# Kernel tuning notes

Hardware: AMD Instinct MI355X
Metric: run time of the kernel (lower is better)

## Reference

```python
import jax, jax.numpy as jnp
import numpy as np

EPS = 1e-5
GROUPS = 8


def setup_inputs() -> dict:
    key = jax.random.key(0)
    ks = jax.random.split(key, 6)
    C = 512
    B, H, W = 4, 64, 64
    s = 1.0 / np.sqrt(C)
    return {
        "x": jax.random.normal(ks[0], (B, C, H, W), dtype=jnp.float32),
        "gn_gamma": jnp.ones((C,), jnp.float32),
        "gn_beta": jnp.zeros((C,), jnp.float32),
        "wq": jax.random.normal(ks[1], (C, C), jnp.float32) * s,
        "bq": jnp.zeros((C,), jnp.float32),
        "wk": jax.random.normal(ks[2], (C, C), jnp.float32) * s,
        "bk": jnp.zeros((C,), jnp.float32),
        "wv": jax.random.normal(ks[3], (C, C), jnp.float32) * s,
        "bv": jnp.zeros((C,), jnp.float32),
        "wp": jax.random.normal(ks[4], (C, C), jnp.float32) * s,
        "bp": jnp.zeros((C,), jnp.float32),
    }


def _group_norm(x, gamma, beta):
    b, c, h, w = x.shape
    xg = x.reshape(b, GROUPS, c // GROUPS, h, w)
    mu = xg.mean(axis=(2, 3, 4), keepdims=True)
    var = xg.var(axis=(2, 3, 4), keepdims=True)
    xn = ((xg - mu) * jax.lax.rsqrt(var + EPS)).reshape(b, c, h, w)
    return xn * gamma[None, :, None, None] + beta[None, :, None, None]


def _conv1x1(x, w, b):
    # 1x1 conv == channel-mixing matmul: [O,C] x [B,C,H,W] -> [B,O,H,W]
    return jnp.einsum('oc,bchw->bohw', w, x) + b[None, :, None, None]


def reference(x, gn_gamma, gn_beta, wq, bq, wk, bk, wv, bv, wp, bp):
    b, c, h, w = x.shape
    xn = _group_norm(x, gn_gamma, gn_beta)  # note: residual uses normalized x, as in source
    q = _conv1x1(xn, wq, bq).reshape(b, c, h * w)
    k = _conv1x1(xn, wk, bk).reshape(b, c, h * w)
    v = _conv1x1(xn, wv, bv).reshape(b, c, h * w)
    scale = jnp.asarray(c, x.dtype) ** 0.5
    attn = jnp.einsum('bci,bcj->bij', q, k) / scale  # [b, hw, hw]
    attn = jax.nn.softmax(attn, axis=2)
    out = jnp.einsum('bij,bcj->bci', attn, v).reshape(b, c, h, w)
    out = _conv1x1(out, wp, bp)
    return xn + out
```

## Files before the change

### kernel.cpp

```cpp
#include <hip/hip_runtime.h>
#include <hip/hip_bf16.h>


typedef unsigned short u16;
typedef unsigned char u8;
typedef __bf16 bf16x8 __attribute__((ext_vector_type(8)));
typedef float f32x4 __attribute__((ext_vector_type(4)));
typedef int i32x4 __attribute__((ext_vector_type(4)));
typedef int i32x8 __attribute__((ext_vector_type(8)));
typedef unsigned short u16x4 __attribute__((ext_vector_type(4)));
typedef unsigned short u16x8 __attribute__((ext_vector_type(8)));

#define CDIM 512
#define NPOS 4096
#define NBATCH 4

__device__ __forceinline__ u16 f2bf(float x) {
  union { float f; unsigned u; } c; c.f = x;
  unsigned u = c.u;
  u += 0x7fffu + ((u >> 16) & 1u);
  return (u16)(u >> 16);
}
__device__ __forceinline__ float bf2f(u16 h) {
  union { unsigned u; float f; } c; c.u = ((unsigned)h) << 16;
  return c.f;
}
__device__ __forceinline__ unsigned pk4_fp8(float a, float b, float c, float d) {
  unsigned v = __builtin_amdgcn_cvt_pk_fp8_f32(a, b, 0, false);
  v = __builtin_amdgcn_cvt_pk_fp8_f32(c, d, v, true);
  return v;
}

__device__ __forceinline__ void async16(const u16* g, u16* l) {
  __builtin_amdgcn_global_load_lds(
      (const __attribute__((address_space(1))) unsigned int*)g,
      (__attribute__((address_space(3))) unsigned int*)l, 16, 0, 0);
}
__device__ __forceinline__ void async16b(const u8* g, u8* l) {
  __builtin_amdgcn_global_load_lds(
      (const __attribute__((address_space(1))) unsigned int*)g,
      (__attribute__((address_space(3))) unsigned int*)l, 16, 0, 0);
}

__device__ __forceinline__ void drain_barrier() {
  asm volatile("s_waitcnt vmcnt(0)" ::: "memory");
  __builtin_amdgcn_s_barrier();
}

__device__ __forceinline__ float wred_sum(float v) {
#pragma unroll
  for (int o = 32; o > 0; o >>= 1) v += __shfl_xor(v, o, 64);
  return v;
}

__global__ __launch_bounds__(256) void gn_partial(const float* __restrict__ x,
                                                  float* __restrict__ stats) {
  int gidx = blockIdx.x >> 3;
  int slice = blockIdx.x & 7;
  const float4* src = (const float4*)x + (long)gidx * 65536 + (long)slice * 8192;
  float s = 0.f, ss = 0.f;
  for (int i = threadIdx.x; i < 8192; i += 256) {
    float4 v = src[i];
    s  += v.x + v.y + v.z + v.w;
    ss += v.x * v.x + v.y * v.y + v.z * v.z + v.w * v.w;
  }
  s = wred_sum(s); ss = wred_sum(ss);
  __shared__ float r1[4], r2[4];
  int lane = threadIdx.x & 63, wave = threadIdx.x >> 6;
  if (lane == 0) { r1[wave] = s; r2[wave] = ss; }
  __syncthreads();
  if (threadIdx.x == 0) {
    atomicAdd(&stats[gidx * 2 + 0], r1[0] + r1[1] + r1[2] + r1[3]);
    atomicAdd(&stats[gidx * 2 + 1], r2[0] + r2[1] + r2[2] + r2[3]);
  }
}

__global__ __launch_bounds__(256) void norm_trans(const float* __restrict__ x,
                                                  const float* __restrict__ stats,
                                                  const float* __restrict__ gamma,
                                                  const float* __restrict__ beta,
                                                  u16* __restrict__ xnb,
                                                  u16* __restrict__ xnT) {
  __shared__ float tile[32][33];
  int b = blockIdx.z, c0 = blockIdx.y * 32, p0 = blockIdx.x * 32;
  int g = (b << 3) + (c0 >> 6);
  float cnt = 1.f / 262144.f;
  float mu = stats[g * 2 + 0] * cnt;
  float ms = stats[g * 2 + 1] * cnt;
  float rstd = rsqrtf(ms - mu * mu + 1e-5f);
  int tp = threadIdx.x & 31, tc = threadIdx.x >> 5;
#pragma unroll
  for (int r = 0; r < 4; r++) {
    int cl = tc + r * 8;
    int c = c0 + cl;
    long idx = ((long)(b * CDIM + c)) * NPOS + p0 + tp;
    float v = (x[idx] - mu) * rstd * gamma[c] + beta[c];
    xnb[idx] = f2bf(v);
    tile[cl][tp] = v;
  }
  __syncthreads();
#pragma unroll
  for (int r = 0; r < 4; r++) {
    int pl = tc + r * 8, cl = tp;
    xnT[((long)(b * NPOS + p0 + pl)) * CDIM + c0 + cl] = f2bf(tile[cl][pl]);
  }
}

__global__ __launch_bounds__(256) void cvt4(const float* __restrict__ a, const float* __restrict__ b,
                                            const float* __restrict__ c, const float* __restrict__ d,
                                            u16* __restrict__ oa, u16* __restrict__ ob,
                                            u16* __restrict__ oc, u16* __restrict__ od) {
  int i = blockIdx.x * 256 + threadIdx.x;
  if (blockIdx.y == 3) {
    int m = i >> 9, k = i & 511;
    u16 v = f2bf(d[i]);
    od[m * 1024 + k] = v;
    od[m * 1024 + 512 + k] = v;
    return;
  }
  const float* src; u16* dst;
  switch (blockIdx.y) {
    case 0: src = a; dst = oa; break;
    case 1: src = b; dst = ob; break;
    default: src = c; dst = oc; break;
  }
  dst[i] = f2bf(src[i]);
}

template <int MODE, int BN>
__global__ __launch_bounds__(BN * 2, 2) void gemm_bt(
    const u16* __restrict__ A, const u16* __restrict__ B,
    void* __restrict__ Cp, const float* __restrict__ bias,
    const float* __restrict__ bias1, const u16* __restrict__ residb,
    const float* __restrict__ laux,
    int N, int K, int lda, int ldb,
    long sA, long sB, long sC, long sR) {
  __shared__ u16 Asm[2][128 * 64];
  __shared__ u16 Bsm[2][BN * 64];
  constexpr int NT = BN * 2;
  constexpr int STEP = NT / 8;
  int bz = blockIdx.z;
  A += (long)bz * sA;
  B += (long)bz * sB;
  int bm = blockIdx.y, bn = blockIdx.x;
  int tid = threadIdx.x;
  int lane = tid & 63, wave = tid >> 6;
  int wm = (wave & 1) * 64, wn = (wave >> 1) * 64;

  int row0 = tid >> 3;
  int ko = (tid & 7) * 8;
  int kos = ko ^ ((row0 & 7) * 8);
  f32x4 acc[4][4] = {};
  int row16 = lane & 15;
  int kq = (lane >> 4) * 8;

  auto stage = [&](int buf, int k0) {
#pragma unroll
    for (int r = 0; r < 128 / STEP; r++) {
      int row = row0 + r * STEP;
      async16(A + (long)(bm * 128 + row) * lda + k0 + kos, &Asm[buf][row * 64 + ko]);
    }
#pragma unroll
    for (int r = 0; r < BN / STEP; r++) {
      int row = row0 + r * STEP;
      async16(B + (long)(bn * BN + row) * ldb + k0 + kos, &Bsm[buf][row * 64 + ko]);
    }
  };

  stage(0, 0);
  drain_barrier();
  int cur = 0;
  for (int k0 = 0; k0 < K; k0 += 64) {
    if (k0 + 64 < K) stage(cur ^ 1, k0 + 64);
#pragma unroll
    for (int s2 = 0; s2 < 2; s2++) {
      bf16x8 af[4], bfr[4];
#pragma unroll
      for (int i = 0; i < 4; i++) {
        int row = wm + i * 16 + row16;
        af[i] = *(const bf16x8*)&Asm[cur][row * 64 + ((s2 * 32 + kq) ^ ((row & 7) * 8))];
      }
#pragma unroll
      for (int j = 0; j < 4; j++) {
        int row = wn + j * 16 + row16;
        bfr[j] = *(const bf16x8*)&Bsm[cur][row * 64 + ((s2 * 32 + kq) ^ ((row & 7) * 8))];
      }
      __builtin_amdgcn_s_setprio(1);
#pragma unroll
      for (int i = 0; i < 4; i++)
#pragma unroll
        for (int j = 0; j < 4; j++)
          acc[i][j] = __builtin_amdgcn_mfma_f32_16x16x32_bf16(bfr[j], af[i], acc[i][j], 0, 0, 0);
      __builtin_amdgcn_s_setprio(0);
    }
    drain_barrier();
    cur ^= 1;
  }

  int mcol = lane & 15, rb = (lane >> 4) * 4;
  long zC = (long)bz * sC;
#pragma unroll
  for (int i = 0; i < 4; i++) {
    int gm = bm * 128 + wm + i * 16 + mcol;
    float bm_add = 0.f;
    if constexpr (MODE == 4 || MODE == 5) bm_add = bias[gm];
#pragma unroll
    for (int j = 0; j < 4; j++) {
      int gn0 = bn * BN + wn + j * 16 + rb;
      long off = zC + (long)gm * N + gn0;
      float v[4];
#pragma unroll
      for (int r = 0; r < 4; r++) v[r] = acc[i][j][r];
      if constexpr (MODE == 0) {
        const float* bb = (gn0 < 512) ? (bias + gn0) : (bias1 + (gn0 - 512));
#pragma unroll
        for (int r = 0; r < 4; r++) v[r] += bb[r];
        *(unsigned*)&((u8*)Cp)[off] = pk4_fp8(v[0], v[1], v[2], v[3]);
      }
      if constexpr (MODE == 4) {
        f32x4 lv = *(const f32x4*)&laux[bz * NPOS + gn0];
        u16x4 rv = *(const u16x4*)&residb[(long)bz * sR + (long)gm * N + gn0];
        f32x4 o;
#pragma unroll
        for (int r = 0; r < 4; r++) o[r] = v[r] / lv[r] + bm_add + bf2f(rv[r]);
        *(f32x4*)&((float*)Cp)[off] = o;
      }
      if constexpr (MODE == 5) {
#pragma unroll
        for (int r = 0; r < 4; r++) v[r] += bm_add;
        *(unsigned*)&((u8*)Cp)[off] = pk4_fp8(v[0], v[1], v[2], v[3]);
      }
    }
  }
}

__global__ __launch_bounds__(256, 2) void smx_gemm(const u8* __restrict__ QKf8,
                                                   u8* __restrict__ P,
                                                   float* __restrict__ l,
                                                   float scale) {
  __shared__ u8 Asm[2][128 * 128];
  __shared__ u8 Bsm[2][128 * 128];
  int bz = blockIdx.z;
  const u8* Ab = QKf8 + (long)bz * 4194304;
  const u8* Bb = Ab + 512;
  int bm = blockIdx.y, bn = blockIdx.x;
  int tid = threadIdx.x, lane = tid & 63, wave = tid >> 6;
  int wm = (wave & 1) * 64, wn = (wave >> 1) * 64;
  int m16 = lane & 15, q = lane >> 4;
  int lrow8 = lane >> 3, lch = lane & 7;

  f32x4 acc[4][4] = {};

  auto stage = [&](int buf, int k0) {
#pragma unroll
    for (int r = 0; r < 4; r++) {
      int row = (wave * 4 + r) * 8 + lrow8;
      int ch = lch ^ (row & 7);
      async16b(Ab + (long)(bm * 128 + row) * 1024 + k0 + ch * 16, &Asm[buf][row * 128 + lch * 16]);
      async16b(Bb + (long)(bn * 128 + row) * 1024 + k0 + ch * 16, &Bsm[buf][row * 128 + lch * 16]);
    }
  };

  stage(0, 0);
  drain_barrier();
  int cur = 0;
  for (int t = 0; t < 4; t++) {
    if (t < 3) stage(cur ^ 1, (t + 1) * 128);
    i32x8 af[4], bf[4];
#pragma unroll
    for (int i = 0; i < 4; i++) {
      int row = wm + i * 16 + m16;
      int sw = (row & 7) * 16;
      i32x4 lo = *(const i32x4*)&Asm[cur][row * 128 + ((q * 32) ^ sw)];
      i32x4 hi = *(const i32x4*)&Asm[cur][row * 128 + ((q * 32 + 16) ^ sw)];
      af[i] = __builtin_shufflevector(lo, hi, 0, 1, 2, 3, 4, 5, 6, 7);
    }
#pragma unroll
    for (int j = 0; j < 4; j++) {
      int row = wn + j * 16 + m16;
      int sw = (row & 7) * 16;
      i32x4 lo = *(const i32x4*)&Bsm[cur][row * 128 + ((q * 32) ^ sw)];
      i32x4 hi = *(const i32x4*)&Bsm[cur][row * 128 + ((q * 32 + 16) ^ sw)];
      bf[j] = __builtin_shufflevector(lo, hi, 0, 1, 2, 3, 4, 5, 6, 7);
    }
    __builtin_amdgcn_s_setprio(1);
#pragma unroll
    for (int i = 0; i < 4; i++)
#pragma unroll
      for (int j = 0; j < 4; j++)
        acc[i][j] = __builtin_amdgcn_mfma_scale_f32_16x16x128_f8f6f4(
            bf[j], af[i], acc[i][j], 0, 0, 0, 0x7F7F7F7F, 0, 0x7F7F7F7F);
    __builtin_amdgcn_s_setprio(0);
    drain_barrier();
    cur ^= 1;
  }

  long zC = (long)bz * 16777216;
  float rsum[4] = {0.f, 0.f, 0.f, 0.f};
#pragma unroll
  for (int i = 0; i < 4; i++) {
    int gi = bm * 128 + wm + i * 16 + m16;
#pragma unroll
    for (int j = 0; j < 4; j++) {
      int gj = bn * 128 + wn + j * 16 + q * 4;
      float v[4];
#pragma unroll
      for (int r = 0; r < 4; r++) { v[r] = __expf(acc[i][j][r] * scale); rsum[i] += v[r]; }
      *(unsigned*)&P[zC + (long)gi * 4096 + gj] = pk4_fp8(v[0], v[1], v[2], v[3]);
    }
  }
#pragma unroll
  for (int i = 0; i < 4; i++) {
    rsum[i] += __shfl_xor(rsum[i], 16, 64);
    rsum[i] += __shfl_xor(rsum[i], 32, 64);
  }
  if (lane < 16) {
    int base = bz * NPOS + bm * 128 + wm + m16;
#pragma unroll
    for (int i = 0; i < 4; i++)
      atomicAdd(&l[base + i * 16], rsum[i]);
  }
}

__global__ __launch_bounds__(256, 2) void hgemm_mx(const u8* __restrict__ P,
                                                   const u8* __restrict__ V,
                                                   u16* __restrict__ part) {
  __shared__ u8 Asm[2][128 * 128];
  __shared__ u8 Bsm[2][128 * 128];
  int z = blockIdx.z;
  int bz = z >> 1, sp = z & 1;
  const u8* Ab = P + (long)bz * 16777216 + sp * 2048;
  const u8* Bb = V + (long)bz * 2097152 + sp * 2048;
  int bm = blockIdx.y, bn = blockIdx.x;
  int tid = threadIdx.x, lane = tid & 63, wave = tid >> 6;
  int wm = (wave & 1) * 64, wn = (wave >> 1) * 64;
  int m16 = lane & 15, q = lane >> 4;
  int lrow8 = lane >> 3, lch = lane & 7;

  f32x4 acc[4][4] = {};

  auto stage = [&](int buf, int k0) {
#pragma unroll
    for (int r = 0; r < 4; r++) {
      int row = (wave * 4 + r) * 8 + lrow8;
      int ch = lch ^ (row & 7);
      async16b(Ab + (long)(bm * 128 + row) * 4096 + k0 + ch * 16, &Asm[buf][row * 128 + lch * 16]);
      async16b(Bb + (long)(bn * 128 + row) * 4096 + k0 + ch * 16, &Bsm[buf][row * 128 + lch * 16]);
    }
  };

  stage(0, 0);
  drain_barrier();
  int cur = 0;
  for (int t = 0; t < 16; t++) {
    if (t < 15) stage(cur ^ 1, (t + 1) * 128);
    i32x8 af[4], bf[4];
#pragma unroll
    for (int i = 0; i < 4; i++) {
      int row = wm + i * 16 + m16;
      int sw = (row & 7) * 16;
      i32x4 lo = *(const i32x4*)&Asm[cur][row * 128 + ((q * 32) ^ sw)];
      i32x4 hi = *(const i32x4*)&Asm[cur][row * 128 + ((q * 32 + 16) ^ sw)];
      af[i] = __builtin_shufflevector(lo, hi, 0, 1, 2, 3, 4, 5, 6, 7);
    }
#pragma unroll
    for (int j = 0; j < 4; j++) {
      int row = wn + j * 16 + m16;
      int sw = (row & 7) * 16;
      i32x4 lo = *(const i32x4*)&Bsm[cur][row * 128 + ((q * 32) ^ sw)];
      i32x4 hi = *(const i32x4*)&Bsm[cur][row * 128 + ((q * 32 + 16) ^ sw)];
      bf[j] = __builtin_shufflevector(lo, hi, 0, 1, 2, 3, 4, 5, 6, 7);
    }
    __builtin_amdgcn_s_setprio(1);
#pragma unroll
    for (int i = 0; i < 4; i++)
#pragma unroll
      for (int j = 0; j < 4; j++)
        acc[i][j] = __builtin_amdgcn_mfma_scale_f32_16x16x128_f8f6f4(
            bf[j], af[i], acc[i][j], 0, 0, 0, 0x7F7F7F7F, 0, 0x7F7F7F7F);
    __builtin_amdgcn_s_setprio(0);
    drain_barrier();
    cur ^= 1;
  }

  long zC = (long)bz * 4194304 + sp * 512;
#pragma unroll
  for (int i = 0; i < 4; i++) {
    int gi = bm * 128 + wm + i * 16 + m16;
#pragma unroll
    for (int j = 0; j < 4; j++) {
      int gc = bn * 128 + wn + j * 16 + q * 4;
      u16x4 o;
#pragma unroll
      for (int r = 0; r < 4; r++) o[r] = f2bf(acc[i][j][r]);
      *(u16x4*)&part[zC + (long)gi * 1024 + gc] = o;
    }
  }
}

extern "C" void kernel_launch(void* const* d_in, const int* in_sizes, int n_in,
                              void* d_out, int out_size, void* d_ws, size_t ws_size,
                              hipStream_t stream) {
  const float* x     = (const float*)d_in[0];
  const float* gamma = (const float*)d_in[1];
  const float* beta  = (const float*)d_in[2];
  const float* wq = (const float*)d_in[3];
  const float* bq = (const float*)d_in[4];
  const float* wk = (const float*)d_in[5];
  const float* bk = (const float*)d_in[6];
  const float* wv = (const float*)d_in[7];
  const float* bv = (const float*)d_in[8];
  const float* wp = (const float*)d_in[9];
  const float* bp = (const float*)d_in[10];
  float* out = (float*)d_out;

  char* W = (char*)d_ws;
  float* stats = (float*)(W + 0);
  float* l     = (float*)(W + 256);
  u16* xnb  = (u16*)(W + 65792);
  u16* xnT  = (u16*)(W + 16843008);
  u16* wqkb = (u16*)(W + 33620224);
  u16* wvb  = (u16*)(W + 34668800);
  u16* wpd  = (u16*)(W + 35193088);
  u8*  QKf8 = (u8*)(W + 37290240);
  u8*  Vf8  = (u8*)(W + 54067456);
  u16* part = (u16*)(W + 62456064);
  u8*  SP   = (u8*)(W + 96010496);
  (void)in_sizes; (void)n_in; (void)out_size; (void)ws_size;

  hipMemsetAsync(W, 0, 65792, stream);
  gn_partial<<<256, 256, 0, stream>>>(x, stats);
  norm_trans<<<dim3(128, 16, 4), 256, 0, stream>>>(x, stats, gamma, beta, xnb, xnT);
  cvt4<<<dim3(1024, 4), 256, 0, stream>>>(wq, wk, wv, wp, wqkb, wqkb + 262144, wvb, wpd);

  const long NC = (long)NPOS * CDIM;
  const long CN = (long)CDIM * NPOS;
  const float scale = 0.044194173824159216f;

  gemm_bt<0, 128><<<dim3(8, 128, 1), 256, 0, stream>>>(xnT, wqkb, QKf8, bq, bk, nullptr, nullptr,
      1024, CDIM, CDIM, CDIM, 0, 0, 0, 0);
  gemm_bt<5, 128><<<dim3(32, 4, 4), 256, 0, stream>>>(wvb, xnT, Vf8, bv, nullptr, nullptr, nullptr,
      NPOS, CDIM, CDIM, CDIM, 0, NC, CN, 0);
  smx_gemm<<<dim3(32, 32, NBATCH), 256, 0, stream>>>(QKf8, SP, l, scale);
  hgemm_mx<<<dim3(4, 32, 8), 256, 0, stream>>>(SP, Vf8, part);
  gemm_bt<4, 128><<<dim3(32, 4, 4), 256, 0, stream>>>(wpd, part, (void*)out, bp, nullptr, xnb, l,
      NPOS, 1024, 1024, 1024, 0, (long)NPOS * 1024, CN, CN);
}
```

Baseline: 322.4 us.

## Merge attention GEMMs into one 256x256-tile MX kernel with 4-stage pipeline

Replaces the separate QK-softmax and PV fp8 GEMM kernels with one templated kernel. It uses 512-thread blocks, 256x256 output tiles, and 32x32x64 scaled MFMA instead of 16x16x128. Loads go through a 4-slot async LDS ring with explicit vmcnt waits, replacing the double buffer with a full drain each step. The aim is more data reuse per tile and better overlap of loads with MFMA. In exchange it needs 128KB of LDS for one block per CU, larger accumulators, and fewer blocks in the grid (e.g. 256 blocks for PV), which risks poor CU occupancy.

```diff
diff --git a/kernel.cpp b/kernel.cpp
--- a/kernel.cpp
+++ b/kernel.cpp
@@ -6,6 +6,7 @@
 typedef unsigned char u8;
 typedef __bf16 bf16x8 __attribute__((ext_vector_type(8)));
 typedef float f32x4 __attribute__((ext_vector_type(4)));
+typedef float f32x16 __attribute__((ext_vector_type(16)));
 typedef int i32x4 __attribute__((ext_vector_type(4)));
 typedef int i32x8 __attribute__((ext_vector_type(8)));
 typedef unsigned short u16x4 __attribute__((ext_vector_type(4)));
@@ -234,166 +235,135 @@
   }
 }
 
-__global__ __launch_bounds__(256, 2) void smx_gemm(const u8* __restrict__ QKf8,
-                                                   u8* __restrict__ P,
-                                                   float* __restrict__ l,
-                                                   float scale) {
-  __shared__ u8 Asm[2][128 * 128];
-  __shared__ u8 Bsm[2][128 * 128];
-  int bz = blockIdx.z;
-  const u8* Ab = QKf8 + (long)bz * 4194304;
-  const u8* Bb = Ab + 512;
-  int bm = blockIdx.y, bn = blockIdx.x;
-  int tid = threadIdx.x, lane = tid & 63, wave = tid >> 6;
-  int wm = (wave & 1) * 64, wn = (wave >> 1) * 64;
-  int m16 = lane & 15, q = lane >> 4;
-  int lrow8 = lane >> 3, lch = lane & 7;
-
-  f32x4 acc[4][4] = {};
-
-  auto stage = [&](int buf, int k0) {
-#pragma unroll
-    for (int r = 0; r < 4; r++) {
-      int row = (wave * 4 + r) * 8 + lrow8;
-      int ch = lch ^ (row & 7);
-      async16b(Ab + (long)(bm * 128 + row) * 1024 + k0 + ch * 16, &Asm[buf][row * 128 + lch * 16]);
-      async16b(Bb + (long)(bn * 128 + row) * 1024 + k0 + ch * 16, &Bsm[buf][row * 128 + lch * 16]);
+template <int MODE, int TSTEPS, int LDAB>
+__global__ __launch_bounds__(512, 1) void mx_gemm(
+    const u8* __restrict__ Abase, const u8* __restrict__ Bbase,
+    void* __restrict__ Out, float* __restrict__ l, float scale) {
+  __shared__ u8 S[4][2][16384];
+  int tid = threadIdx.x, lane = tid & 63, w = tid >> 6;
+  int wm = (w & 1) * 128, wn = (w >> 1) * 64;
+  int bm = blockIdx.y, bn = blockIdx.x, bz = blockIdx.z;
+  int l31 = lane & 31, h = lane >> 5;
+
+  const u8 *Ab, *Bb;
+  if constexpr (MODE == 0) {
+    Ab = Abase + (long)bz * 4194304;
+    Bb = Ab + 512;
+  } else {
+    int b = bz >> 1, sp = bz & 1;
+    Ab = Abase + (long)b * 16777216 + sp * 2048;
+    Bb = Bbase + (long)b * 2097152 + sp * 2048;
+  }
+
+  f32x16 acc[4][2] = {};
+
+  auto stage = [&](int slot, int k0) {
+    u8* dA = &S[slot][0][0];
+    u8* dB = &S[slot][1][0];
+#pragma unroll
+    for (int half = 0; half < 2; half++) {
+      int z = tid + half * 512;
+      int ldsrow = z >> 3;
+      int gch = (z & 7) ^ (ldsrow & 7);
+      int row = ldsrow * 2 + (gch >> 2);
+      int c16 = gch & 3;
+      async16b(Ab + (long)(bm * 256 + row) * LDAB + k0 + c16 * 16, dA + z * 16);
+      async16b(Bb + (long)(bn * 256 + row) * LDAB + k0 + c16 * 16, dB + z * 16);
     }
   };
 
   stage(0, 0);
-  drain_barrier();
-  int cur = 0;
-  for (int t = 0; t < 4; t++) {
-    if (t < 3) stage(cur ^ 1, (t + 1) * 128);
-    i32x8 af[4], bf[4];
-#pragma unroll
-    for (int i = 0; i < 4; i++) {
-      int row = wm + i * 16 + m16;
-      int sw = (row & 7) * 16;
-      i32x4 lo = *(const i32x4*)&Asm[cur][row * 128 + ((q * 32) ^ sw)];
-      i32x4 hi = *(const i32x4*)&Asm[cur][row * 128 + ((q * 32 + 16) ^ sw)];
-      af[i] = __builtin_shufflevector(lo, hi, 0, 1, 2, 3, 4, 5, 6, 7);
-    }
-#pragma unroll
-    for (int j = 0; j < 4; j++) {
-      int row = wn + j * 16 + m16;
-      int sw = (row & 7) * 16;
-      i32x4 lo = *(const i32x4*)&Bsm[cur][row * 128 + ((q * 32) ^ sw)];
-      i32x4 hi = *(const i32x4*)&Bsm[cur][row * 128 + ((q * 32 + 16) ^ sw)];
-      bf[j] = __builtin_shufflevector(lo, hi, 0, 1, 2, 3, 4, 5, 6, 7);
+  stage(1, 64);
+  stage(2, 128);
+
+  for (int t = 0; t < TSTEPS; t++) {
+    if (t < TSTEPS - 2)      { asm volatile("s_waitcnt vmcnt(8)" ::: "memory"); }
+    else if (t == TSTEPS - 2){ asm volatile("s_waitcnt vmcnt(4)" ::: "memory"); }
+    else                     { asm volatile("s_waitcnt vmcnt(0)" ::: "memory"); }
+    __builtin_amdgcn_s_barrier();
+    __builtin_amdgcn_sched_barrier(0);
+    if (t + 3 < TSTEPS) stage((t + 3) & 3, (t + 3) * 64);
+
+    int slot = t & 3;
+    const u8* As = &S[slot][0][0];
+    const u8* Bs = &S[slot][1][0];
+    i32x8 af[4], bf[2];
+#pragma unroll
+    for (int mr = 0; mr < 4; mr++) {
+      int r = wm + mr * 32 + l31;
+      int lr = r >> 1, sw = lr & 7;
+      int g0 = (r & 1) * 4 + h * 2;
+      i32x4 lo = *(const i32x4*)&As[lr * 128 + ((g0 ^ sw) * 16)];
+      i32x4 hi = *(const i32x4*)&As[lr * 128 + (((g0 + 1) ^ sw) * 16)];
+      af[mr] = __builtin_shufflevector(lo, hi, 0, 1, 2, 3, 4, 5, 6, 7);
+    }
+#pragma unroll
+    for (int nr = 0; nr < 2; nr++) {
+      int r = wn + nr * 32 + l31;
+      int lr = r >> 1, sw = lr & 7;
+      int g0 = (r & 1) * 4 + h * 2;
+      i32x4 lo = *(const i32x4*)&Bs[lr * 128 + ((g0 ^ sw) * 16)];
+      i32x4 hi = *(const i32x4*)&Bs[lr * 128 + (((g0 + 1) ^ sw) * 16)];
+      bf[nr] = __builtin_shufflevector(lo, hi, 0, 1, 2, 3, 4, 5, 6, 7);
     }
     __builtin_amdgcn_s_setprio(1);
 #pragma unroll
-    for (int i = 0; i < 4; i++)
-#pragma unroll
-      for (int j = 0; j < 4; j++)
-        acc[i][j] = __builtin_amdgcn_mfma_scale_f32_16x16x128_f8f6f4(
-            bf[j], af[i], acc[i][j], 0, 0, 0, 0x7F7F7F7F, 0, 0x7F7F7F7F);
+    for (int mr = 0; mr < 4; mr++)
+#pragma unroll
+      for (int nr = 0; nr < 2; nr++)
+        acc[mr][nr] = __builtin_amdgcn_mfma_scale_f32_32x32x64_f8f6f4(
+            bf[nr], af[mr], acc[mr][nr], 0, 0, 0, 0x7F7F7F7F, 0, 0x7F7F7F7F);
     __builtin_amdgcn_s_setprio(0);
-    drain_barrier();
-    cur ^= 1;
-  }
-
-  long zC = (long)bz * 16777216;
-  float rsum[4] = {0.f, 0.f, 0.f, 0.f};
-#pragma unroll
-  for (int i = 0; i < 4; i++) {
-    int gi = bm * 128 + wm + i * 16 + m16;
-#pragma unroll
-    for (int j = 0; j < 4; j++) {
-      int gj = bn * 128 + wn + j * 16 + q * 4;
-      float v[4];
-#pragma unroll
-      for (int r = 0; r < 4; r++) { v[r] = __expf(acc[i][j][r] * scale); rsum[i] += v[r]; }
-      *(unsigned*)&P[zC + (long)gi * 4096 + gj] = pk4_fp8(v[0], v[1], v[2], v[3]);
-    }
-  }
-#pragma unroll
-  for (int i = 0; i < 4; i++) {
-    rsum[i] += __shfl_xor(rsum[i], 16, 64);
-    rsum[i] += __shfl_xor(rsum[i], 32, 64);
-  }
-  if (lane < 16) {
-    int base = bz * NPOS + bm * 128 + wm + m16;
-#pragma unroll
-    for (int i = 0; i < 4; i++)
-      atomicAdd(&l[base + i * 16], rsum[i]);
-  }
-}
-
-__global__ __launch_bounds__(256, 2) void hgemm_mx(const u8* __restrict__ P,
-                                                   const u8* __restrict__ V,
-                                                   u16* __restrict__ part) {
-  __shared__ u8 Asm[2][128 * 128];
-  __shared__ u8 Bsm[2][128 * 128];
-  int z = blockIdx.z;
-  int bz = z >> 1, sp = z & 1;
-  const u8* Ab = P + (long)bz * 16777216 + sp * 2048;
-  const u8* Bb = V + (long)bz * 2097152 + sp * 2048;
-  int bm = blockIdx.y, bn = blockIdx.x;
-  int tid = threadIdx.x, lane = tid & 63, wave = tid >> 6;
-  int wm = (wave & 1) * 64, wn = (wave >> 1) * 64;
-  int m16 = lane & 15, q = lane >> 4;
-  int lrow8 = lane >> 3, lch = lane & 7;
-
-  f32x4 acc[4][4] = {};
-
-  auto stage = [&](int buf, int k0) {
-#pragma unroll
-    for (int r = 0; r < 4; r++) {
-      int row = (wave * 4 + r) * 8 + lrow8;
-      int ch = lch ^ (row & 7);
-      async16b(Ab + (long)(bm * 128 + row) * 4096 + k0 + ch * 16, &Asm[buf][row * 128 + lch * 16]);
-      async16b(Bb + (long)(bn * 128 + row) * 4096 + k0 + ch * 16, &Bsm[buf][row * 128 + lch * 16]);
-    }
-  };
-
-  stage(0, 0);
-  drain_barrier();
-  int cur = 0;
-  for (int t = 0; t < 16; t++) {
-    if (t < 15) stage(cur ^ 1, (t + 1) * 128);
-    i32x8 af[4], bf[4];
-#pragma unroll
-    for (int i = 0; i < 4; i++) {
-      int row = wm + i * 16 + m16;
-      int sw = (row & 7) * 16;
-      i32x4 lo = *(const i32x4*)&Asm[cur][row * 128 + ((q * 32) ^ sw)];
-      i32x4 hi = *(const i32x4*)&Asm[cur][row * 128 + ((q * 32 + 16) ^ sw)];
-      af[i] = __builtin_shufflevector(lo, hi, 0, 1, 2, 3, 4, 5, 6, 7);
-    }
-#pragma unroll
-    for (int j = 0; j < 4; j++) {
-      int row = wn + j * 16 + m16;
-      int sw = (row & 7) * 16;
-      i32x4 lo = *(const i32x4*)&Bsm[cur][row * 128 + ((q * 32) ^ sw)];
-      i32x4 hi = *(const i32x4*)&Bsm[cur][row * 128 + ((q * 32 + 16) ^ sw)];
-      bf[j] = __builtin_shufflevector(lo, hi, 0, 1, 2, 3, 4, 5, 6, 7);
-    }
-    __builtin_amdgcn_s_setprio(1);
-#pragma unroll
-    for (int i = 0; i < 4; i++)
-#pragma unroll
-      for (int j = 0; j < 4; j++)
-        acc[i][j] = __builtin_amdgcn_mfma_scale_f32_16x16x128_f8f6f4(
-            bf[j], af[i], acc[i][j], 0, 0, 0, 0x7F7F7F7F, 0, 0x7F7F7F7F);
-    __builtin_amdgcn_s_setprio(0);
-    drain_barrier();
-    cur ^= 1;
-  }
-
-  long zC = (long)bz * 4194304 + sp * 512;
-#pragma unroll
-  for (int i = 0; i < 4; i++) {
-    int gi = bm * 128 + wm + i * 16 + m16;
-#pragma unroll
-    for (int j = 0; j < 4; j++) {
-      int gc = bn * 128 + wn + j * 16 + q * 4;
-      u16x4 o;
-#pragma unroll
-      for (int r = 0; r < 4; r++) o[r] = f2bf(acc[i][j][r]);
-      *(u16x4*)&part[zC + (long)gi * 1024 + gc] = o;
+  }
+
+  if constexpr (MODE == 0) {
+    long zC = (long)bz * 16777216;
+    u8* P = (u8*)Out;
+    float rsum[4] = {0.f, 0.f, 0.f, 0.f};
+#pragma unroll
+    for (int mr = 0; mr < 4; mr++) {
+      int gi = bm * 256 + wm + mr * 32 + l31;
+#pragma unroll
+      for (int nr = 0; nr < 2; nr++) {
+        int jb = bn * 256 + wn + nr * 32 + h * 4;
+#pragma unroll
+        for (int g = 0; g < 4; g++) {
+          float v0 = __expf(acc[mr][nr][g * 4 + 0] * scale);
+          float v1 = __expf(acc[mr][nr][g * 4 + 1] * scale);
+          float v2 = __expf(acc[mr][nr][g * 4 + 2] * scale);
+          float v3 = __expf(acc[mr][nr][g * 4 + 3] * scale);
+          rsum[mr] += v0 + v1 + v2 + v3;
+          *(unsigned*)&P[zC + (long)gi * 4096 + jb + 8 * g] = pk4_fp8(v0, v1, v2, v3);
+        }
+      }
+    }
+#pragma unroll
+    for (int mr = 0; mr < 4; mr++) rsum[mr] += __shfl_xor(rsum[mr], 32, 64);
+    if (lane < 32) {
+      int base = bz * NPOS + bm * 256 + wm + l31;
+#pragma unroll
+      for (int mr = 0; mr < 4; mr++) atomicAdd(&l[base + mr * 32], rsum[mr]);
+    }
+  } else {
+    int b = bz >> 1, sp = bz & 1;
+    long zC = (long)b * 4194304 + sp * 512;
+    u16* part = (u16*)Out;
+#pragma unroll
+    for (int mr = 0; mr < 4; mr++) {
+      int gi = bm * 256 + wm + mr * 32 + l31;
+#pragma unroll
+      for (int nr = 0; nr < 2; nr++) {
+        int cb = bn * 256 + wn + nr * 32 + h * 4;
+#pragma unroll
+        for (int g = 0; g < 4; g++) {
+          u16x4 o;
+          o[0] = f2bf(acc[mr][nr][g * 4 + 0]);
+          o[1] = f2bf(acc[mr][nr][g * 4 + 1]);
+          o[2] = f2bf(acc[mr][nr][g * 4 + 2]);
+          o[3] = f2bf(acc[mr][nr][g * 4 + 3]);
+          *(u16x4*)&part[zC + (long)gi * 1024 + cb + 8 * g] = o;
+        }
+      }
     }
   }
 }
@@ -441,8 +411,8 @@
       1024, CDIM, CDIM, CDIM, 0, 0, 0, 0);
   gemm_bt<5, 128><<<dim3(32, 4, 4), 256, 0, stream>>>(wvb, xnT, Vf8, bv, nullptr, nullptr, nullptr,
       NPOS, CDIM, CDIM, CDIM, 0, NC, CN, 0);
-  smx_gemm<<<dim3(32, 32, NBATCH), 256, 0, stream>>>(QKf8, SP, l, scale);
-  hgemm_mx<<<dim3(4, 32, 8), 256, 0, stream>>>(SP, Vf8, part);
+  mx_gemm<0, 8, 1024><<<dim3(16, 16, NBATCH), 512, 0, stream>>>(QKf8, nullptr, SP, l, scale);
+  mx_gemm<1, 32, 4096><<<dim3(2, 16, 8), 512, 0, stream>>>(SP, Vf8, part, nullptr, 0.f);
   gemm_bt<4, 128><<<dim3(32, 4, 4), 256, 0, stream>>>(wpd, part, (void*)out, bp, nullptr, xnb, l,
       NPOS, 1024, 1024, 1024, 0, (long)NPOS * 1024, CN, CN);
 }
```

Measured after the change: 323.3 us. About the same (+0.3%).
